# Kernel optimization log

Measured on AMD Instinct MI355X. Metric: run time of the kernel, lower is better.

## Reference

```python
import jax, jax.numpy as jnp
import numpy as np

B, T, D, H = 2, 4096, 768, 12
DH = D // H


def setup_inputs() -> dict:
    key = jax.random.key(0)
    ks = jax.random.split(key, 4)
    x = jax.random.normal(ks[0], (B, T, D), dtype=jnp.float32)
    Wqkv = jax.random.normal(ks[1], (D, 3 * D), dtype=jnp.float32) * (D ** -0.5)
    bqkv = jnp.zeros((3 * D,), dtype=jnp.float32)
    Wproj = jax.random.normal(ks[2], (D, D), dtype=jnp.float32) * (D ** -0.5)
    bproj = jnp.zeros((D,), dtype=jnp.float32)
    return {"x": x, "Wqkv": Wqkv, "bqkv": bqkv, "Wproj": Wproj, "bproj": bproj}


def reference(x, Wqkv, bqkv, Wproj, bproj):
    b, t, c = x.shape
    qkv = x @ Wqkv + bqkv                      # [B,T,3D]
    qkv = qkv.reshape(b, t, H, 3 * DH)
    q, k, v = jnp.split(qkv, 3, axis=-1)       # each [B,T,H,DH]
    q = q.transpose(0, 2, 1, 3)                # [B,H,T,DH]
    k = k.transpose(0, 2, 1, 3)
    v = v.transpose(0, 2, 1, 3)
    att = jnp.einsum('bhqd,bhkd->bhqk', q, k) / (DH ** 0.5)  # [B,H,T,T]
    mask = jnp.tril(jnp.ones((t, t), dtype=bool))
    att = jnp.where(mask, att, jnp.float32(-1e9))
    att = jax.nn.softmax(att, axis=-1)
    out = jnp.einsum('bhqk,bhkd->bhqd', att, v)  # [B,H,T,DH]
    out = out.transpose(0, 2, 1, 3).reshape(b, t, c)
    return out @ Wproj + bproj
```

## Files before the change

### kernel.cpp

```cpp
#include <hip/hip_runtime.h>

typedef unsigned short u16;
typedef unsigned int u32;
typedef __bf16 bf16x8 __attribute__((ext_vector_type(8)));
typedef float f32x4 __attribute__((ext_vector_type(4)));
typedef float f32x16 __attribute__((ext_vector_type(16)));
typedef u16 u16x4 __attribute__((ext_vector_type(4)));
typedef u32 u32x2 __attribute__((ext_vector_type(2)));
typedef u32 u32x4 __attribute__((ext_vector_type(4)));

#define QSCALE 0.18033688011112042f

static __device__ __forceinline__ u16 f2bf(float f) {
  __bf16 h = (__bf16)f;
  return __builtin_bit_cast(u16, h);
}

static __device__ __forceinline__ u32 pk2(float a, float b) {
  return (u32)f2bf(a) | ((u32)f2bf(b) << 16);
}

static __device__ __forceinline__ void gl_lds16(const void* g, void* l) {
  __builtin_amdgcn_global_load_lds(
      (const __attribute__((address_space(1))) unsigned int*)g,
      (__attribute__((address_space(3))) unsigned int*)l, 16, 0, 0);
}

static __device__ __forceinline__ void wait_vmcnt8() {
  asm volatile("s_waitcnt vmcnt(8)" ::: "memory");
  __builtin_amdgcn_sched_barrier(0);
}
static __device__ __forceinline__ void wait_vmcnt0() {
  asm volatile("s_waitcnt vmcnt(0)" ::: "memory");
  __builtin_amdgcn_sched_barrier(0);
}
static __device__ __forceinline__ void barrier_mem() {
  asm volatile("s_barrier" ::: "memory");
  __builtin_amdgcn_sched_barrier(0);
}

static __device__ __forceinline__ f32x16 zero16() {
  f32x16 z;
#pragma unroll
  for (int i = 0; i < 16; ++i) z[i] = 0.f;
  return z;
}

__global__ void k_cvt(const float* __restrict__ in, u16* __restrict__ out, int n4) {
  int i = blockIdx.x * 256 + threadIdx.x;
  if (i < n4) {
    f32x4 f = ((const f32x4*)in)[i];
    u16x4 u = { f2bf(f[0]), f2bf(f[1]), f2bf(f[2]), f2bf(f[3]) };
    ((u16x4*)out)[i] = u;
  }
}

__global__ void k_transpose_cvt(const float* __restrict__ in, u16* __restrict__ out,
                                int R, int C) {
  __shared__ float tile[32][33];
  const int c0 = blockIdx.x * 32, r0 = blockIdx.y * 32;
  const int tx = threadIdx.x, ty = threadIdx.y;
#pragma unroll
  for (int i = 0; i < 4; ++i)
    tile[ty + i * 8][tx] = in[(size_t)(r0 + ty + i * 8) * C + c0 + tx];
  __syncthreads();
#pragma unroll
  for (int i = 0; i < 4; ++i)
    out[(size_t)(c0 + ty + i * 8) * R + r0 + tx] = f2bf(tile[tx][ty + i * 8]);
}

static __device__ __forceinline__ void gemm_core(const u16* __restrict__ Ag,
                                                 const u16* __restrict__ Btg,
                                                 int K, int m0, int n0,
                                                 u16* As, u16* Bs,
                                                 f32x4 acc[4][4]) {
  const int tid = threadIdx.x;
  const int lane = tid & 63;
  const int wid = tid >> 6;
  const int wm = wid >> 1, wn = wid & 1;
  const int l16 = lane & 15, lg = lane >> 4;

  for (int kt = 0; kt < K; kt += 64) {
    __syncthreads();
#pragma unroll
    for (int i = 0; i < 4; ++i) {
      int chunk = i * 256 + tid;
      int row = chunk >> 3;
      int lcb = ((chunk & 7) << 4) ^ ((row & 7) << 4);
      gl_lds16(Ag + (size_t)(m0 + row) * K + kt + (lcb >> 1),
               As + ((i * 256 + wid * 64) << 3));
    }
#pragma unroll
    for (int i = 0; i < 4; ++i) {
      int chunk = i * 256 + tid;
      int row = chunk >> 3;
      int lcb = ((chunk & 7) << 4) ^ ((row & 7) << 4);
      gl_lds16(Btg + (size_t)(n0 + row) * K + kt + (lcb >> 1),
               Bs + ((i * 256 + wid * 64) << 3));
    }
    __syncthreads();

#pragma unroll
    for (int ks = 0; ks < 2; ++ks) {
      bf16x8 af[4], bfr[4];
#pragma unroll
      for (int mi = 0; mi < 4; ++mi) {
        int row = wm * 64 + mi * 16 + l16;
        int off = row * 128 + ((ks * 64 + (lg << 4)) ^ ((row & 7) << 4));
        af[mi] = *(const bf16x8*)((const char*)As + off);
      }
#pragma unroll
      for (int ni = 0; ni < 4; ++ni) {
        int row = wn * 64 + ni * 16 + l16;
        int off = row * 128 + ((ks * 64 + (lg << 4)) ^ ((row & 7) << 4));
        bfr[ni] = *(const bf16x8*)((const char*)Bs + off);
      }
#pragma unroll
      for (int mi = 0; mi < 4; ++mi)
#pragma unroll
        for (int ni = 0; ni < 4; ++ni)
          acc[mi][ni] = __builtin_amdgcn_mfma_f32_16x16x32_bf16(
              af[mi], bfr[ni], acc[mi][ni], 0, 0, 0);
    }
  }
}

__global__ __launch_bounds__(256) void k_gemm_qkv(
    const u16* __restrict__ A, const u16* __restrict__ Bt,
    const float* __restrict__ bias, u16* __restrict__ Q, u16* __restrict__ Kb,
    u16* __restrict__ Vt) {
  __shared__ __align__(16) u16 As[128 * 64];
  __shared__ __align__(16) u16 Bs[128 * 64];
  const int m0 = blockIdx.y * 128, n0 = blockIdx.x * 128;
  const f32x4 fz = {0.f, 0.f, 0.f, 0.f};
  f32x4 acc[4][4];
#pragma unroll
  for (int mi = 0; mi < 4; ++mi)
#pragma unroll
    for (int ni = 0; ni < 4; ++ni) acc[mi][ni] = fz;

  gemm_core(A, Bt, 768, m0, n0, As, Bs, acc);

  const int tid = threadIdx.x, lane = tid & 63, wid = tid >> 6;
  const int wm = wid >> 1, wn = wid & 1, l16 = lane & 15, lg = lane >> 4;
#pragma unroll
  for (int mi = 0; mi < 4; ++mi)
#pragma unroll
    for (int ni = 0; ni < 4; ++ni) {
      int n = n0 + wn * 64 + ni * 16 + l16;
      float bi = bias[n];
      int h = n / 192;
      int rr = n - h * 192;
      int m0w = m0 + wm * 64 + mi * 16 + lg * 4;
      int bb = m0w >> 12, t0 = m0w & 4095;
      size_t base = ((size_t)(bb * 12 + h) * 4096 + t0) * 64;
      if (rr < 64) {
#pragma unroll
        for (int r = 0; r < 4; ++r)
          Q[base + (size_t)r * 64 + rr] = f2bf((acc[mi][ni][r] + bi) * QSCALE);
      } else if (rr < 128) {
#pragma unroll
        for (int r = 0; r < 4; ++r)
          Kb[base + (size_t)r * 64 + rr - 64] = f2bf(acc[mi][ni][r] + bi);
      } else {
        u16x4 vv;
#pragma unroll
        for (int r = 0; r < 4; ++r) vv[r] = f2bf(acc[mi][ni][r] + bi);
        *(u16x4*)(Vt + ((size_t)(bb * 12 + h) * 64 + (rr - 128)) * 4096 + t0) = vv;
      }
    }
}

__global__ __launch_bounds__(256) void k_gemm_proj(
    const u16* __restrict__ A, const u16* __restrict__ Bt,
    const float* __restrict__ bias, float* __restrict__ out) {
  __shared__ __align__(16) u16 As[128 * 64];
  __shared__ __align__(16) u16 Bs[128 * 64];
  const int m0 = blockIdx.y * 128, n0 = blockIdx.x * 128;
  const f32x4 fz = {0.f, 0.f, 0.f, 0.f};
  f32x4 acc[4][4];
#pragma unroll
  for (int mi = 0; mi < 4; ++mi)
#pragma unroll
    for (int ni = 0; ni < 4; ++ni) acc[mi][ni] = fz;

  gemm_core(A, Bt, 768, m0, n0, As, Bs, acc);

  const int tid = threadIdx.x, lane = tid & 63, wid = tid >> 6;
  const int wm = wid >> 1, wn = wid & 1, l16 = lane & 15, lg = lane >> 4;
#pragma unroll
  for (int mi = 0; mi < 4; ++mi)
#pragma unroll
    for (int ni = 0; ni < 4; ++ni) {
      int n = n0 + wn * 64 + ni * 16 + l16;
      float bi = bias[n];
#pragma unroll
      for (int r = 0; r < 4; ++r) {
        int m = m0 + wm * 64 + mi * 16 + lg * 4 + r;
        out[(size_t)m * 768 + n] = acc[mi][ni][r] + bi;
      }
    }
}

__global__ __launch_bounds__(128) void k_attn(const u16* __restrict__ Qg,
                                              const u16* __restrict__ Kg,
                                              const u16* __restrict__ Vtg,
                                              u16* __restrict__ Og) {
  __shared__ __align__(16) u16 Ks[2][64 * 64];
  __shared__ __align__(16) u16 Vs[2][64 * 64];
  const int bid = blockIdx.x;
  const int xcd = bid & 7;
  const int u = bid >> 3;
  const int s = u & 31;
  const int rnd = u >> 5;
  const int bh = xcd * 3 + (rnd >> 1);
  const int jX = (rnd & 1) ? s : (63 - s);
  const int tid = threadIdx.x;
  const int lane = tid & 63;
  const int wid = tid >> 6;
  const int l32 = lane & 31;
  const int hi = lane >> 5;
  const int rxor = (l32 & 7) << 4;
  const size_t qk_base = (size_t)bh * (4096 * 64);
  const size_t vt_base = (size_t)bh * (64 * 4096);
  const int b = bh / 12, h = bh - b * 12;

  const int q0w = jX * 64 + wid * 32;
  const int qrow = q0w + l32;
  const int nkt = jX + 1;

  int coK[4], coVa[4], coVb[4];
#pragma unroll
  for (int st = 0; st < 4; ++st) coK[st] = (st * 32 + hi * 16) ^ rxor;
#pragma unroll
  for (int ks = 0; ks < 4; ++ks) {
    coVa[ks] = (ks * 32 + hi * 8) ^ rxor;
    coVb[ks] = (ks * 32 + 16 + hi * 8) ^ rxor;
  }
  const int rb0 = l32 * 128, rb1 = (32 + l32) * 128;

  const int trow = tid >> 3;
  const int tcol = ((((tid & 7) << 4) ^ ((trow & 7) << 4)) >> 1);
  const int tdst = tid << 3;
  const u16* kp0 = Kg + qk_base + (size_t)trow * 64 + tcol;
  const u16* kp1 = kp0 + (size_t)16 * 64;
  const u16* kp2 = kp0 + (size_t)32 * 64;
  const u16* kp3 = kp0 + (size_t)48 * 64;
  const u16* vq0 = Vtg + vt_base + (size_t)trow * 4096 + tcol;
  const u16* vq1 = vq0 + (size_t)16 * 4096;
  const u16* vq2 = vq0 + (size_t)32 * 4096;
  const u16* vq3 = vq0 + (size_t)48 * 4096;

  auto stage = [&](u16* Kd, u16* Vd) {
    gl_lds16(kp0, Kd + tdst);
    gl_lds16(kp1, Kd + 1024 + tdst);
    gl_lds16(kp2, Kd + 2048 + tdst);
    gl_lds16(kp3, Kd + 3072 + tdst);
    gl_lds16(vq0, Vd + tdst);
    gl_lds16(vq1, Vd + 1024 + tdst);
    gl_lds16(vq2, Vd + 2048 + tdst);
    gl_lds16(vq3, Vd + 3072 + tdst);
    kp0 += 4096; kp1 += 4096; kp2 += 4096; kp3 += 4096;
    vq0 += 64; vq1 += 64; vq2 += 64; vq3 += 64;
  };

  bf16x8 qb[4];
#pragma unroll
  for (int st = 0; st < 4; ++st)
    qb[st] = *(const bf16x8*)(Qg + qk_base + (size_t)qrow * 64 + st * 16 + hi * 8);

  f32x16 o0 = zero16(), o1 = zero16();
  float mrun = -3.0e38f, lrun = 0.f;

  stage(Ks[0], Vs[0]);

  int cur = 0;
  for (int kt = 0; kt < nkt; ++kt) {
    if (kt + 1 < nkt) {
      stage(Ks[cur ^ 1], Vs[cur ^ 1]);
      wait_vmcnt8();
    } else {
      wait_vmcnt0();
    }
    barrier_mem();

    const bool diag = (kt == nkt - 1);
    const bool halfskip = diag && (wid == 0);
    const char* Kbp = (const char*)Ks[cur];
    const char* Vb = (const char*)Vs[cur];

    f32x16 s0 = zero16(), s1 = zero16();
    __builtin_amdgcn_s_setprio(1);
#pragma unroll
    for (int st = 0; st < 4; ++st) {
      bf16x8 ka0 = *(const bf16x8*)(Kbp + rb0 + coK[st]);
      s0 = __builtin_amdgcn_mfma_f32_32x32x16_bf16(ka0, qb[st], s0, 0, 0, 0);
    }
    if (!halfskip) {
#pragma unroll
      for (int st = 0; st < 4; ++st) {
        bf16x8 ka1 = *(const bf16x8*)(Kbp + rb1 + coK[st]);
        s1 = __builtin_amdgcn_mfma_f32_32x32x16_bf16(ka1, qb[st], s1, 0, 0, 0);
      }
    }
    __builtin_amdgcn_s_setprio(0);

    if (diag) {
      const int kbase = kt * 64 + 4 * hi;
#pragma unroll
      for (int r = 0; r < 16; ++r) {
        int kpv = kbase + (r & 3) + 8 * (r >> 2);
        s0[r] = (kpv > qrow) ? -3.0e38f : s0[r];
        if (!halfskip) s1[r] = (kpv + 32 > qrow) ? -3.0e38f : s1[r];
      }
    }

    float m8[8];
#pragma unroll
    for (int r = 0; r < 8; ++r) {
      float v = fmaxf(s0[r], s0[r + 8]);
      if (!halfskip) v = fmaxf(v, fmaxf(s1[r], s1[r + 8]));
      m8[r] = v;
    }
    float mx = fmaxf(fmaxf(fmaxf(m8[0], m8[1]), fmaxf(m8[2], m8[3])),
                     fmaxf(fmaxf(m8[4], m8[5]), fmaxf(m8[6], m8[7])));
    mx = fmaxf(mx, __shfl_xor(mx, 32, 64));

    if (__ballot(mx > mrun + 8.0f) != 0ull) {
      float mnew = fmaxf(mrun, mx);
      float al = __builtin_amdgcn_exp2f(mrun - mnew);
      o0 *= al;
      o1 *= al;
      lrun *= al;
      mrun = mnew;
    }

#pragma unroll
    for (int r = 0; r < 16; ++r) {
      s0[r] = __builtin_amdgcn_exp2f(s0[r] - mrun);
      if (!halfskip) s1[r] = __builtin_amdgcn_exp2f(s1[r] - mrun);
    }

    float a8[8];
#pragma unroll
    for (int r = 0; r < 8; ++r) {
      float v = s0[r] + s0[r + 8];
      if (!halfskip) v += s1[r] + s1[r + 8];
      a8[r] = v;
    }
    float rs = ((a8[0] + a8[1]) + (a8[2] + a8[3])) +
               ((a8[4] + a8[5]) + (a8[6] + a8[7]));
    rs += __shfl_xor(rs, 32, 64);
    lrun += rs;

    __builtin_amdgcn_s_setprio(1);
#pragma unroll
    for (int ks = 0; ks < 4; ++ks) {
      if (ks >= 2 && halfskip) continue;
      const f32x16& P = (ks >= 2) ? s1 : s0;
      const int base = (ks & 1) * 8;
      u32x4 w = { pk2(P[base + 0], P[base + 1]), pk2(P[base + 2], P[base + 3]),
                  pk2(P[base + 4], P[base + 5]), pk2(P[base + 6], P[base + 7]) };
      bf16x8 pbk = __builtin_bit_cast(bf16x8, w);
      u32x2 q0 = *(const u32x2*)(Vb + rb0 + coVa[ks]);
      u32x2 q1 = *(const u32x2*)(Vb + rb0 + coVb[ks]);
      u32x4 av = {q0[0], q0[1], q1[0], q1[1]};
      bf16x8 va0 = __builtin_bit_cast(bf16x8, av);
      o0 = __builtin_amdgcn_mfma_f32_32x32x16_bf16(va0, pbk, o0, 0, 0, 0);
      u32x2 p0 = *(const u32x2*)(Vb + rb1 + coVa[ks]);
      u32x2 p1 = *(const u32x2*)(Vb + rb1 + coVb[ks]);
      u32x4 bv = {p0[0], p0[1], p1[0], p1[1]};
      bf16x8 va1 = __builtin_bit_cast(bf16x8, bv);
      o1 = __builtin_amdgcn_mfma_f32_32x32x16_bf16(va1, pbk, o1, 0, 0, 0);
    }
    __builtin_amdgcn_s_setprio(0);

    barrier_mem();
    cur ^= 1;
  }

  float inv = 1.0f / lrun;
  u16* orow = Og + ((size_t)b * 4096 + qrow) * 768 + h * 64;
#pragma unroll
  for (int gg = 0; gg < 4; ++gg) {
    u16x4 v0, v1;
#pragma unroll
    for (int i = 0; i < 4; ++i) {
      v0[i] = f2bf(o0[4 * gg + i] * inv);
      v1[i] = f2bf(o1[4 * gg + i] * inv);
    }
    *(u16x4*)(orow + 8 * gg + 4 * hi) = v0;
    *(u16x4*)(orow + 32 + 8 * gg + 4 * hi) = v1;
  }
}

extern "C" void kernel_launch(void* const* d_in, const int* in_sizes, int n_in,
                              void* d_out, int out_size, void* d_ws, size_t ws_size,
                              hipStream_t stream) {
  const float* x = (const float*)d_in[0];
  const float* Wqkv = (const float*)d_in[1];
  const float* bqkv = (const float*)d_in[2];
  const float* Wproj = (const float*)d_in[3];
  const float* bproj = (const float*)d_in[4];
  float* out = (float*)d_out;

  char* ws = (char*)d_ws;
  u16* Xbf = (u16*)(ws + 0);
  u16* WqkvT = (u16*)(ws + 12582912);
  u16* WprojT = (u16*)(ws + 16121856);
  u16* Q = (u16*)(ws + 17301504);
  u16* K = (u16*)(ws + 29884416);
  u16* Vt = (u16*)(ws + 42467328);
  u16* O = (u16*)(ws + 55050240);

  k_cvt<<<6144, 256, 0, stream>>>(x, Xbf, 1572864);
  k_transpose_cvt<<<dim3(72, 24), dim3(32, 8), 0, stream>>>(Wqkv, WqkvT, 768, 2304);
  k_transpose_cvt<<<dim3(24, 24), dim3(32, 8), 0, stream>>>(Wproj, WprojT, 768, 768);
  k_gemm_qkv<<<dim3(18, 64), 256, 0, stream>>>(Xbf, WqkvT, bqkv, Q, K, Vt);
  k_attn<<<1536, 128, 0, stream>>>(Q, K, Vt, O);
  k_gemm_proj<<<dim3(6, 64), 256, 0, stream>>>(O, WprojT, bproj, out);
}
```

Baseline: 214.6 us.

## Pair low and high causal query tiles per block to share K/V loads

Each attention block now handles two query tiles, t and 63−t, and runs both against the same staged K/V tiles. This balances causal work across blocks and halves the grid to 768. It also reuses each K/V tile load for both query tiles. The row-sum cross-lane shuffle moves to the end of the kernel, which cuts per-iteration shuffles. In exchange the kernel carries roughly double the accumulator registers and has fewer blocks, which can lower occupancy.

New measurement: 291.6 us. +35.9%, slower.

```diff
diff --git a/kernel.cpp b/kernel.cpp
--- a/kernel.cpp
+++ b/kernel.cpp
@@ -213,8 +213,9 @@
   const int u = bid >> 3;
   const int s = u & 31;
   const int rnd = u >> 5;
-  const int bh = xcd * 3 + (rnd >> 1);
-  const int jX = (rnd & 1) ? s : (63 - s);
+  const int bh = xcd * 3 + rnd;
+  const int t = (rnd & 1) ? (31 - s) : s;
+  const int qtL = t, qtH = 63 - t;
   const int tid = threadIdx.x;
   const int lane = tid & 63;
   const int wid = tid >> 6;
@@ -225,9 +226,9 @@
   const size_t vt_base = (size_t)bh * (64 * 4096);
   const int b = bh / 12, h = bh - b * 12;
 
-  const int q0w = jX * 64 + wid * 32;
-  const int qrow = q0w + l32;
-  const int nkt = jX + 1;
+  const int qrowL = qtL * 64 + wid * 32 + l32;
+  const int qrowH = qtH * 64 + wid * 32 + l32;
+  const int nkt = qtH + 1;
 
   int coK[4], coVa[4], coVb[4];
 #pragma unroll
@@ -264,31 +265,20 @@
     vq0 += 64; vq1 += 64; vq2 += 64; vq3 += 64;
   };
 
-  bf16x8 qb[4];
-#pragma unroll
-  for (int st = 0; st < 4; ++st)
-    qb[st] = *(const bf16x8*)(Qg + qk_base + (size_t)qrow * 64 + st * 16 + hi * 8);
-
-  f32x16 o0 = zero16(), o1 = zero16();
-  float mrun = -3.0e38f, lrun = 0.f;
-
-  stage(Ks[0], Vs[0]);
-
-  int cur = 0;
-  for (int kt = 0; kt < nkt; ++kt) {
-    if (kt + 1 < nkt) {
-      stage(Ks[cur ^ 1], Vs[cur ^ 1]);
-      wait_vmcnt8();
-    } else {
-      wait_vmcnt0();
-    }
-    barrier_mem();
-
-    const bool diag = (kt == nkt - 1);
-    const bool halfskip = diag && (wid == 0);
-    const char* Kbp = (const char*)Ks[cur];
-    const char* Vb = (const char*)Vs[cur];
-
+  bf16x8 qbL[4], qbH[4];
+#pragma unroll
+  for (int st = 0; st < 4; ++st) {
+    qbL[st] = *(const bf16x8*)(Qg + qk_base + (size_t)qrowL * 64 + st * 16 + hi * 8);
+    qbH[st] = *(const bf16x8*)(Qg + qk_base + (size_t)qrowH * 64 + st * 16 + hi * 8);
+  }
+
+  f32x16 oL0 = zero16(), oL1 = zero16(), oH0 = zero16(), oH1 = zero16();
+  float mrunL = -3.0e38f, lrunL = 0.f;
+  float mrunH = -3.0e38f, lrunH = 0.f;
+
+  auto unit = [&](const char* Kbp, const char* Vb, const bf16x8* qb, int qrowU,
+                  f32x16& o0, f32x16& o1, float& mrun, float& lrun,
+                  int kt, bool diag, bool halfskip) {
     f32x16 s0 = zero16(), s1 = zero16();
     __builtin_amdgcn_s_setprio(1);
 #pragma unroll
@@ -310,8 +300,8 @@
 #pragma unroll
       for (int r = 0; r < 16; ++r) {
         int kpv = kbase + (r & 3) + 8 * (r >> 2);
-        s0[r] = (kpv > qrow) ? -3.0e38f : s0[r];
-        if (!halfskip) s1[r] = (kpv + 32 > qrow) ? -3.0e38f : s1[r];
+        s0[r] = (kpv > qrowU) ? -3.0e38f : s0[r];
+        if (!halfskip) s1[r] = (kpv + 32 > qrowU) ? -3.0e38f : s1[r];
       }
     }
 
@@ -348,10 +338,8 @@
       if (!halfskip) v += s1[r] + s1[r + 8];
       a8[r] = v;
     }
-    float rs = ((a8[0] + a8[1]) + (a8[2] + a8[3])) +
-               ((a8[4] + a8[5]) + (a8[6] + a8[7]));
-    rs += __shfl_xor(rs, 32, 64);
-    lrun += rs;
+    lrun += ((a8[0] + a8[1]) + (a8[2] + a8[3])) +
+            ((a8[4] + a8[5]) + (a8[6] + a8[7]));
 
     __builtin_amdgcn_s_setprio(1);
 #pragma unroll
@@ -374,23 +362,64 @@
       o1 = __builtin_amdgcn_mfma_f32_32x32x16_bf16(va1, pbk, o1, 0, 0, 0);
     }
     __builtin_amdgcn_s_setprio(0);
+  };
+
+  stage(Ks[0], Vs[0]);
+
+  int cur = 0;
+  for (int kt = 0; kt < nkt; ++kt) {
+    if (kt + 1 < nkt) {
+      stage(Ks[cur ^ 1], Vs[cur ^ 1]);
+      wait_vmcnt8();
+    } else {
+      wait_vmcnt0();
+    }
+    barrier_mem();
+
+    const char* Kbp = (const char*)Ks[cur];
+    const char* Vb = (const char*)Vs[cur];
+
+    unit(Kbp, Vb, qbH, qrowH, oH0, oH1, mrunH, lrunH,
+         kt, kt == qtH, (kt == qtH) && (wid == 0));
+    if (kt <= qtL)
+      unit(Kbp, Vb, qbL, qrowL, oL0, oL1, mrunL, lrunL,
+           kt, kt == qtL, (kt == qtL) && (wid == 0));
 
     barrier_mem();
     cur ^= 1;
   }
 
-  float inv = 1.0f / lrun;
-  u16* orow = Og + ((size_t)b * 4096 + qrow) * 768 + h * 64;
-#pragma unroll
-  for (int gg = 0; gg < 4; ++gg) {
-    u16x4 v0, v1;
-#pragma unroll
-    for (int i = 0; i < 4; ++i) {
-      v0[i] = f2bf(o0[4 * gg + i] * inv);
-      v1[i] = f2bf(o1[4 * gg + i] * inv);
-    }
-    *(u16x4*)(orow + 8 * gg + 4 * hi) = v0;
-    *(u16x4*)(orow + 32 + 8 * gg + 4 * hi) = v1;
+  {
+    float lt = lrunL + __shfl_xor(lrunL, 32, 64);
+    float inv = 1.0f / lt;
+    u16* orow = Og + ((size_t)b * 4096 + qrowL) * 768 + h * 64;
+#pragma unroll
+    for (int gg = 0; gg < 4; ++gg) {
+      u16x4 v0, v1;
+#pragma unroll
+      for (int i = 0; i < 4; ++i) {
+        v0[i] = f2bf(oL0[4 * gg + i] * inv);
+        v1[i] = f2bf(oL1[4 * gg + i] * inv);
+      }
+      *(u16x4*)(orow + 8 * gg + 4 * hi) = v0;
+      *(u16x4*)(orow + 32 + 8 * gg + 4 * hi) = v1;
+    }
+  }
+  {
+    float lt = lrunH + __shfl_xor(lrunH, 32, 64);
+    float inv = 1.0f / lt;
+    u16* orow = Og + ((size_t)b * 4096 + qrowH) * 768 + h * 64;
+#pragma unroll
+    for (int gg = 0; gg < 4; ++gg) {
+      u16x4 v0, v1;
+#pragma unroll
+      for (int i = 0; i < 4; ++i) {
+        v0[i] = f2bf(oH0[4 * gg + i] * inv);
+        v1[i] = f2bf(oH1[4 * gg + i] * inv);
+      }
+      *(u16x4*)(orow + 8 * gg + 4 * hi) = v0;
+      *(u16x4*)(orow + 32 + 8 * gg + 4 * hi) = v1;
+    }
   }
 }
 
@@ -417,6 +446,6 @@
   k_transpose_cvt<<<dim3(72, 24), dim3(32, 8), 0, stream>>>(Wqkv, WqkvT, 768, 2304);
   k_transpose_cvt<<<dim3(24, 24), dim3(32, 8), 0, stream>>>(Wproj, WprojT, 768, 768);
   k_gemm_qkv<<<dim3(18, 64), 256, 0, stream>>>(Xbf, WqkvT, bqkv, Q, K, Vt);
-  k_attn<<<1536, 128, 0, stream>>>(Q, K, Vt, O);
+  k_attn<<<768, 128, 0, stream>>>(Q, K, Vt, O);
   k_gemm_proj<<<dim3(6, 64), 256, 0, stream>>>(O, WprojT, bproj, out);
 }
```

## Replace double-buffered K/V LDS staging with single buffer

Applied to the files above, without the earlier changes.

Converts the attention kernel's K/V tile staging from a two-slot ping-pong to a single LDS buffer. Each iteration now loads the tile and waits for it before computing. This halves the shared memory per block, which could allow more resident blocks. In exchange it removes the overlap of global loads with MFMA compute, exposing load latency every iteration.

Result: no change. 211.9 us (-1.2%).

```diff
diff --git a/kernel.cpp b/kernel.cpp
--- a/kernel.cpp
+++ b/kernel.cpp
@@ -26,10 +26,6 @@
       (__attribute__((address_space(3))) unsigned int*)l, 16, 0, 0);
 }
 
-static __device__ __forceinline__ void wait_vmcnt8() {
-  asm volatile("s_waitcnt vmcnt(8)" ::: "memory");
-  __builtin_amdgcn_sched_barrier(0);
-}
 static __device__ __forceinline__ void wait_vmcnt0() {
   asm volatile("s_waitcnt vmcnt(0)" ::: "memory");
   __builtin_amdgcn_sched_barrier(0);
@@ -206,8 +202,8 @@
                                               const u16* __restrict__ Kg,
                                               const u16* __restrict__ Vtg,
                                               u16* __restrict__ Og) {
-  __shared__ __align__(16) u16 Ks[2][64 * 64];
-  __shared__ __align__(16) u16 Vs[2][64 * 64];
+  __shared__ __align__(16) u16 Ks[64 * 64];
+  __shared__ __align__(16) u16 Vs[64 * 64];
   const int bid = blockIdx.x;
   const int xcd = bid & 7;
   const int u = bid >> 3;
@@ -251,15 +247,15 @@
   const u16* vq2 = vq0 + (size_t)32 * 4096;
   const u16* vq3 = vq0 + (size_t)48 * 4096;
 
-  auto stage = [&](u16* Kd, u16* Vd) {
-    gl_lds16(kp0, Kd + tdst);
-    gl_lds16(kp1, Kd + 1024 + tdst);
-    gl_lds16(kp2, Kd + 2048 + tdst);
-    gl_lds16(kp3, Kd + 3072 + tdst);
-    gl_lds16(vq0, Vd + tdst);
-    gl_lds16(vq1, Vd + 1024 + tdst);
-    gl_lds16(vq2, Vd + 2048 + tdst);
-    gl_lds16(vq3, Vd + 3072 + tdst);
+  auto stage = [&]() {
+    gl_lds16(kp0, Ks + tdst);
+    gl_lds16(kp1, Ks + 1024 + tdst);
+    gl_lds16(kp2, Ks + 2048 + tdst);
+    gl_lds16(kp3, Ks + 3072 + tdst);
+    gl_lds16(vq0, Vs + tdst);
+    gl_lds16(vq1, Vs + 1024 + tdst);
+    gl_lds16(vq2, Vs + 2048 + tdst);
+    gl_lds16(vq3, Vs + 3072 + tdst);
     kp0 += 4096; kp1 += 4096; kp2 += 4096; kp3 += 4096;
     vq0 += 64; vq1 += 64; vq2 += 64; vq3 += 64;
   };
@@ -272,22 +268,15 @@
   f32x16 o0 = zero16(), o1 = zero16();
   float mrun = -3.0e38f, lrun = 0.f;
 
-  stage(Ks[0], Vs[0]);
-
-  int cur = 0;
   for (int kt = 0; kt < nkt; ++kt) {
-    if (kt + 1 < nkt) {
-      stage(Ks[cur ^ 1], Vs[cur ^ 1]);
-      wait_vmcnt8();
-    } else {
-      wait_vmcnt0();
-    }
+    stage();
+    wait_vmcnt0();
     barrier_mem();
 
     const bool diag = (kt == nkt - 1);
     const bool halfskip = diag && (wid == 0);
-    const char* Kbp = (const char*)Ks[cur];
-    const char* Vb = (const char*)Vs[cur];
+    const char* Kbp = (const char*)Ks;
+    const char* Vb = (const char*)Vs;
 
     f32x16 s0 = zero16(), s1 = zero16();
     __builtin_amdgcn_s_setprio(1);
@@ -376,7 +365,6 @@
     __builtin_amdgcn_s_setprio(0);
 
     barrier_mem();
-    cur ^= 1;
   }
 
   float inv = 1.0f / lrun;
```
